# Kernel tuning notes

Hardware: AMD Instinct MI355X
Metric: run time of the kernel (lower is better)

Reference implementation:

```python
import jax, jax.numpy as jnp
import numpy as np

H = 1024   # hidden_dim
I = 256    # input_dim
T = 128    # time_step
NW = 4     # input_num (weeks)
N = 100    # stocks = 5 categories * 20
C, G = 5, 20


def gru(x, Wih, Whh, bih, bhh):
    """Torch-style single-layer GRU. x: (B,T,I) batch_first -> (B,T,H). Gate order r,z,n."""
    gx = jnp.einsum('bti,gi->btg', x, Wih) + bih  # (B,T,3H) input projections precomputed
    h0 = jnp.zeros((x.shape[0], Whh.shape[1]), x.dtype)

    def step(h, g):
        gh = h @ Whh.T + bhh
        xr, xz, xn = jnp.split(g, 3, axis=-1)
        hr, hz, hn = jnp.split(gh, 3, axis=-1)
        r = jax.nn.sigmoid(xr + hr)
        z = jax.nn.sigmoid(xz + hz)
        n = jnp.tanh(xn + r * hn)
        h = (1.0 - z) * n + z * h
        return h, h

    _, ys = jax.lax.scan(step, h0, jnp.swapaxes(gx, 0, 1))
    return jnp.swapaxes(ys, 0, 1)


def att_block(x, W, b):
    """AttentionBlock: x (B,T,D); Linear over time axis, softmax over time, weighted sum."""
    xt = jnp.swapaxes(x, 1, 2)                    # (B,D,T)
    probs = jax.nn.softmax(xt @ W.T + b, axis=-1) # (B,D,T)
    probs = jnp.swapaxes(probs, 1, 2)             # (B,T,D)
    return (probs * x).sum(axis=1)                # (B,D)


def gat(x, edges, W, a_s, a_d, bias):
    """PyG GATConv, heads=1, add_self_loops=True, leaky_relu slope 0.2."""
    n = x.shape[0]
    h = x @ W.T                                   # (n,H)
    loop = jnp.arange(n)
    src = jnp.concatenate([edges[0], loop])
    dst = jnp.concatenate([edges[1], loop])
    e = jax.nn.leaky_relu((h @ a_s)[src] + (h @ a_d)[dst], 0.2)
    m = jax.ops.segment_max(e, dst, num_segments=n)
    ex = jnp.exp(e - m[dst])
    s = jax.ops.segment_sum(ex, dst, num_segments=n)
    alpha = ex / s[dst]
    return jax.ops.segment_sum(alpha[:, None] * h[src], dst, num_segments=n) + bias


def setup_inputs() -> dict:
    key = jax.random.key(0)
    ks = iter(jax.random.split(key, 64))
    p = lambda *s: jax.random.normal(next(ks), s, dtype=jnp.float32) * 0.05
    inp = {}
    for i in range(NW):
        inp[f'w{i}'] = jax.random.normal(next(ks), (N, T, I), dtype=jnp.float32)
    inp['inner_edge'] = jax.random.randint(next(ks), (2, 2000), 0, N, dtype=jnp.int32)
    inp['outer_edge'] = jax.random.randint(next(ks), (2, 25), 0, C, dtype=jnp.int32)
    # per-week sequence encoders (stacked)
    inp['enc_Wih'] = p(NW, 3 * H, I); inp['enc_Whh'] = p(NW, 3 * H, H)
    inp['enc_bih'] = p(NW, 3 * H);    inp['enc_bhh'] = p(NW, 3 * H)
    inp['enc_attW'] = p(NW, T, T);    inp['enc_attb'] = p(NW, T)
    # weekly GRU (not batch_first in torch!)
    inp['wk_Wih'] = p(3 * H, H); inp['wk_Whh'] = p(3 * H, H)
    inp['wk_bih'] = p(3 * H);    inp['wk_bhh'] = p(3 * H)
    inp['wkatt_W'] = p(NW, NW); inp['wkatt_b'] = p(NW)
    inp['pool_W'] = p(G, G);    inp['pool_b'] = p(G)
    inp['ig_W'] = p(H, H); inp['ig_as'] = p(H); inp['ig_ad'] = p(H); inp['ig_b'] = p(H)
    inp['cg_W'] = p(H, H); inp['cg_as'] = p(H); inp['cg_ad'] = p(H); inp['cg_b'] = p(H)
    inp['fus_W'] = p(H, 3 * H); inp['fus_b'] = p(H)
    inp['reg_W'] = p(1, H); inp['reg_b'] = p(1)
    inp['cls_W'] = p(1, H); inp['cls_b'] = p(1)
    return inp


def reference(w0, w1, w2, w3, inner_edge, outer_edge,
              enc_Wih, enc_Whh, enc_bih, enc_bhh, enc_attW, enc_attb,
              wk_Wih, wk_Whh, wk_bih, wk_bhh, wkatt_W, wkatt_b,
              pool_W, pool_b, ig_W, ig_as, ig_ad, ig_b,
              cg_W, cg_as, cg_ad, cg_b, fus_W, fus_b,
              reg_W, reg_b, cls_W, cls_b):
    weeks = [w0, w1, w2, w3]
    embs = []
    for i in range(NW):
        seq = gru(weeks[i], enc_Wih[i], enc_Whh[i], enc_bih[i], enc_bhh[i])  # (N,T,H)
        embs.append(att_block(seq, enc_attW[i], enc_attb[i])[:, None, :])    # (N,1,H)
    we = jnp.concatenate(embs, axis=1)                                       # (N,NW,H)
    # torch nn.GRU default seq-major: scans over dim0 (N stocks), batch=NW
    we = jnp.swapaxes(gru(jnp.swapaxes(we, 0, 1), wk_Wih, wk_Whh, wk_bih, wk_bhh), 0, 1)
    wav = att_block(we, wkatt_W, wkatt_b)                                    # (N,H)
    inner = gat(wav, inner_edge, ig_W, ig_as, ig_ad, ig_b).reshape(C, G, -1)
    wav3 = wav.reshape(C, G, -1)
    cat = att_block(wav3, pool_W, pool_b)                                    # (C,H)
    cat = gat(cat, outer_edge, cg_W, cg_as, cg_ad, cg_b)                     # (C,H)
    cat = jnp.broadcast_to(cat[:, None, :], (C, G, cat.shape[-1]))
    f = jnp.concatenate([wav3, cat, inner], axis=-1)                         # (C,G,3H)
    f = jax.nn.relu(f @ fus_W.T + fus_b)
    reg = (f @ reg_W.T + reg_b).reshape(-1)
    cls = jax.nn.sigmoid(f @ cls_W.T + cls_b).reshape(-1)
    return reg, cls
```

## Files before the change

kernel.cpp:

```cpp
#include <hip/hip_runtime.h>
#include <hip/hip_bf16.h>

#define NW 4
#define NST 100
#define TT 128
#define II 256
#define HH 1024
#define H3 3072

typedef _Float16 h8 __attribute__((ext_vector_type(8)));
typedef float f4 __attribute__((ext_vector_type(4)));

__device__ __forceinline__ float sigf(float x) { return 1.0f / (1.0f + __expf(-x)); }
__device__ __forceinline__ float tanhfast(float x) { return 1.0f - 2.0f / (1.0f + __expf(2.0f * x)); }

__device__ __forceinline__ float4 ld_f4_sc1(const float* p) {
    union { unsigned long long u[2]; float4 v; } r;
    r.u[0] = __hip_atomic_load((unsigned long long*)p, __ATOMIC_RELAXED, __HIP_MEMORY_SCOPE_AGENT);
    r.u[1] = __hip_atomic_load((unsigned long long*)p + 1, __ATOMIC_RELAXED, __HIP_MEMORY_SCOPE_AGENT);
    return r.v;
}
__device__ __forceinline__ float ld_f_sc1(const float* p) {
    return __hip_atomic_load((float*)p, __ATOMIC_RELAXED, __HIP_MEMORY_SCOPE_AGENT);
}

__device__ __forceinline__ void spin_wait(unsigned* f, unsigned t) {
    int guard = 0;
    while (__hip_atomic_load(f, __ATOMIC_RELAXED, __HIP_MEMORY_SCOPE_AGENT) <= t) {
        __builtin_amdgcn_s_sleep(1);
        if (++guard > (1 << 20)) break;
    }
}

__global__ void zero_k(float* a, int n) {
    int i = blockIdx.x * 256 + threadIdx.x;
    if (i < n) a[i] = 0.0f;
}

__global__ void convW_k(const float* __restrict__ Whh, const float* __restrict__ Wih,
                        _Float16* __restrict__ Wc) {
    int col = blockIdx.x * 256 + threadIdx.x;
    int r = blockIdx.y;
    int w = blockIdx.z;
    float v = (col < HH) ? Whh[((size_t)w * H3 + r) * HH + col]
                         : Wih[((size_t)w * H3 + r) * II + (col - HH)];
    Wc[((size_t)w * H3 + r) * 1280 + col] = (_Float16)v;
}

__global__ void convWk_k(const float* __restrict__ src, _Float16* __restrict__ dst) {
    int col = blockIdx.x * 256 + threadIdx.x;
    int r = blockIdx.y;
    dst[(size_t)r * HH + col] = (_Float16)src[(size_t)r * HH + col];
}

__global__ void xcvt_k(const float* __restrict__ x0, const float* __restrict__ x1,
                       const float* __restrict__ x2, const float* __restrict__ x3,
                       _Float16* __restrict__ xT) {
    int idx = blockIdx.x * 256 + threadIdx.x;
    int k8 = idx & 31;
    int m  = (idx >> 5) & 127;
    int t  = (idx >> 12) & 127;
    int w  = idx >> 19;
    const float* xw = (w == 0) ? x0 : (w == 1) ? x1 : (w == 2) ? x2 : x3;
    h8 hv = {};
    if (m < NST) {
        const float* s = xw + ((size_t)m * TT + t) * II + k8 * 8;
        float4 fa = *(const float4*)s;
        float4 fb = *(const float4*)(s + 4);
        hv[0] = (_Float16)fa.x; hv[1] = (_Float16)fa.y;
        hv[2] = (_Float16)fa.z; hv[3] = (_Float16)fa.w;
        hv[4] = (_Float16)fb.x; hv[5] = (_Float16)fb.y;
        hv[6] = (_Float16)fb.z; hv[7] = (_Float16)fb.w;
    }
    *(h8*)&xT[(((size_t)w * TT + t) * 128 + m) * II + k8 * 8] = hv;
}

__global__ void wTcvt_k(const float* __restrict__ attW, float* __restrict__ wT) {
    int tp = threadIdx.x;
    int t  = blockIdx.x;
    int w  = blockIdx.y;
    wT[((size_t)w * TT + t) * TT + tp] = attW[((size_t)w * TT + tp) * TT + t];
}

__global__ void convB_k(const float* __restrict__ bih, const float* __restrict__ bhh,
                        float* __restrict__ bc) {
    int j = blockIdx.x * 256 + threadIdx.x;
    int w = blockIdx.y;
    const float* bi = bih + w * H3;
    const float* bh = bhh + w * H3;
    float* o = bc + w * 4096;
    o[j] = bi[j] + bh[j];
    o[1024 + j] = bi[1024 + j] + bh[1024 + j];
    o[2048 + j] = bi[2048 + j];
    o[3072 + j] = bh[2048 + j];
}

#define ENC_LDS_HALFS (40 * 3 * 16 * 32)
#define ENC_LDS_BYTES (ENC_LDS_HALFS * 2)

__global__ __launch_bounds__(256) void enc_fused_k(
    const _Float16* __restrict__ Wc, const float* __restrict__ bc,
    const _Float16* __restrict__ xT,
    _Float16* __restrict__ hhA, _Float16* __restrict__ hhB,
    _Float16* __restrict__ seq, unsigned* flags)
{
    extern __shared__ _Float16 Bs[];

    int id = blockIdx.x;
    int rr = id & 7, qq = id >> 3;
    int w  = rr >> 1;
    int bx = qq * 2 + (rr & 1);
    int j0 = bx * 16;

    const _Float16* Wcw = Wc + (size_t)w * H3 * 1280;
    const float* bcw = bc + w * 4096;
    _Float16* hA = hhA + (size_t)w * 128 * HH;
    _Float16* hB = hhB + (size_t)w * 128 * HH;
    unsigned* fw = flags + (size_t)w * 64 * 16;
    unsigned* genw = flags + (size_t)(256 + w) * 16;

    int tid = threadIdx.x;
    int lane = tid & 63, wi = tid >> 6, quad = lane >> 4, l15 = lane & 15;

    if (tid < 192) {
        int brow = tid >> 2, bseg = tid & 3;
        int g = brow >> 4, jj = brow & 15;
        const _Float16* bsrc =
            Wcw + (size_t)(g * 1024 + j0 + jj) * 1280 + bseg * 8;
        #pragma unroll 8
        for (int c = 0; c < 40; c++) {
            uint4 v = *(const uint4*)(bsrc + c * 32);
            *(uint4*)&Bs[(((size_t)c * 3 + g) * 16 + jj) * 32 + bseg * 8] = v;
        }
    }
    __syncthreads();

    int j = j0 + l15;
    float br = bcw[j], bz = bcw[1024 + j], bni = bcw[2048 + j], bnh = bcw[3072 + j];
    int r0 = wi * 32 + l15, r1 = wi * 32 + 16 + l15;
    float hreg[2][4] = {};

    h8 xb0[8], xb1[8];
    {
        const _Float16* x0p = xT + ((size_t)w * TT) * 128 * II;
        #pragma unroll
        for (int u = 0; u < 8; u++) {
            xb0[u] = *(const h8*)(x0p + (size_t)r0 * II + quad * 8 + u * 32);
            xb1[u] = *(const h8*)(x0p + (size_t)r1 * II + quad * 8 + u * 32);
        }
    }

    for (int t = 0; t < TT; t++) {
        const _Float16* hin = (t & 1) ? hB : hA;
        _Float16* hout = (t & 1) ? hA : hB;
        const _Float16* pA0h = hin + (size_t)r0 * HH + quad * 8;
        const _Float16* pA1h = hin + (size_t)r1 * HH + quad * 8;

        f4 aR[2] = {}, aZ[2] = {}, aNH[2] = {}, aNX[2] = {};

        h8 rb0[12], rb1[12];
        #pragma unroll
        for (int u = 0; u < 12; u++) {
            rb0[u] = *(const h8*)(pA0h + u * 32);
            rb1[u] = *(const h8*)(pA1h + u * 32);
        }

        #pragma unroll
        for (int c = 0; c < 40; c++) {
            h8 a0, a1;
            if (c < 32) {
                int u = c % 12;
                a0 = rb0[u]; a1 = rb1[u];
                int cn = c + 12;
                if (cn < 32) {
                    rb0[u] = *(const h8*)(pA0h + cn * 32);
                    rb1[u] = *(const h8*)(pA1h + cn * 32);
                }
            } else {
                a0 = xb0[c - 32]; a1 = xb1[c - 32];
            }
            const _Float16* bb = &Bs[(size_t)c * 1536];
            h8 bf0 = *(const h8*)&bb[l15 * 32 + quad * 8];
            h8 bf1 = *(const h8*)&bb[512 + l15 * 32 + quad * 8];
            h8 bf2 = *(const h8*)&bb[1024 + l15 * 32 + quad * 8];
            aR[0] = __builtin_amdgcn_mfma_f32_16x16x32_f16(a0, bf0, aR[0], 0, 0, 0);
            aR[1] = __builtin_amdgcn_mfma_f32_16x16x32_f16(a1, bf0, aR[1], 0, 0, 0);
            aZ[0] = __builtin_amdgcn_mfma_f32_16x16x32_f16(a0, bf1, aZ[0], 0, 0, 0);
            aZ[1] = __builtin_amdgcn_mfma_f32_16x16x32_f16(a1, bf1, aZ[1], 0, 0, 0);
            if (c < 32) {
                aNH[0] = __builtin_amdgcn_mfma_f32_16x16x32_f16(a0, bf2, aNH[0], 0, 0, 0);
                aNH[1] = __builtin_amdgcn_mfma_f32_16x16x32_f16(a1, bf2, aNH[1], 0, 0, 0);
            } else {
                aNX[0] = __builtin_amdgcn_mfma_f32_16x16x32_f16(a0, bf2, aNX[0], 0, 0, 0);
                aNX[1] = __builtin_amdgcn_mfma_f32_16x16x32_f16(a1, bf2, aNX[1], 0, 0, 0);
            }
        }

        unsigned pks[2][4];
        #pragma unroll
        for (int mi = 0; mi < 2; mi++) {
            #pragma unroll
            for (int p = 0; p < 4; p++) {
                int row = wi * 32 + mi * 16 + quad * 4 + p;
                float r = sigf(aR[mi][p] + br);
                float z = sigf(aZ[mi][p] + bz);
                float n = tanhfast(aNX[mi][p] + bni + r * (aNH[mi][p] + bnh));
                float hv = (1.f - z) * n + z * hreg[mi][p];
                hreg[mi][p] = hv;
                unsigned short hb = __builtin_bit_cast(unsigned short, (_Float16)hv);
                unsigned ob = __shfl_xor((unsigned)hb, 1);
                unsigned pk = (unsigned)hb | (ob << 16);
                pks[mi][p] = pk;
                if (!(l15 & 1) && t < TT - 1)
                    __hip_atomic_exchange((unsigned*)&hout[(size_t)row * HH + j], pk,
                                          __ATOMIC_RELAXED, __HIP_MEMORY_SCOPE_AGENT);
            }
        }
        if (t < TT - 1) {
            __syncthreads();
            if (tid == 0)
                __hip_atomic_store(&fw[bx * 16], (unsigned)(t + 1),
                                   __ATOMIC_RELAXED, __HIP_MEMORY_SCOPE_AGENT);
        }
        #pragma unroll
        for (int mi = 0; mi < 2; mi++) {
            #pragma unroll
            for (int p = 0; p < 4; p++) {
                int row = wi * 32 + mi * 16 + quad * 4 + p;
                if (!(l15 & 1) && row < NST)
                    __hip_atomic_store(
                        (unsigned*)&seq[(((size_t)w * NST + row) * TT + t) * HH + j],
                        pks[mi][p], __ATOMIC_RELAXED, __HIP_MEMORY_SCOPE_AGENT);
            }
        }
        if (t < TT - 1) {
            const _Float16* xn = xT + ((size_t)w * TT + t + 1) * 128 * II;
            #pragma unroll
            for (int u = 0; u < 8; u++) {
                xb0[u] = *(const h8*)(xn + (size_t)r0 * II + quad * 8 + u * 32);
                xb1[u] = *(const h8*)(xn + (size_t)r1 * II + quad * 8 + u * 32);
            }
            if (bx == 0) {
                if (tid < 64) spin_wait(&fw[tid * 16], (unsigned)t);
                __syncthreads();
                if (tid == 0)
                    __hip_atomic_store(genw, (unsigned)(t + 1),
                                       __ATOMIC_RELAXED, __HIP_MEMORY_SCOPE_AGENT);
            } else {
                if (tid == 0) spin_wait(genw, (unsigned)t);
                __syncthreads();
            }
            __builtin_amdgcn_fence(__ATOMIC_ACQUIRE, "agent");
        }
    }
}

__global__ __launch_bounds__(256) void att1_k(
    const _Float16* __restrict__ seq, const float* __restrict__ wT,
    const float* __restrict__ attb, float* __restrict__ wex)
{
    int d0 = blockIdx.x * 128;
    int n  = blockIdx.y;
    int w  = blockIdx.z;
    __shared__ _Float16 S[128][128];
    __shared__ float PM[16][136];
    int tid = threadIdx.x;
    const _Float16* sp = seq + ((size_t)(w * NST + n) * TT) * HH + d0;
    for (int q = tid; q < 2048; q += 256) {
        int t = q >> 4, seg = q & 15;
        *(h8*)&S[t][seg * 8] = *(const h8*)(sp + (size_t)t * HH + seg * 8);
    }
    __syncthreads();
    int tx = tid & 15, ty = tid >> 4;
    const float* Wg = wT + (size_t)w * TT * TT;
    float acc[8][8];
    #pragma unroll
    for (int i = 0; i < 8; i++) {
        float b = attb[w * TT + ty * 8 + i];
        for (int j = 0; j < 8; j++) acc[i][j] = b;
    }
    for (int t = 0; t < 128; t++) {
        float wv[8], sv[8];
        float4 wa = *(const float4*)&Wg[(size_t)t * TT + ty * 8];
        float4 wb = *(const float4*)&Wg[(size_t)t * TT + ty * 8 + 4];
        wv[0] = wa.x; wv[1] = wa.y; wv[2] = wa.z; wv[3] = wa.w;
        wv[4] = wb.x; wv[5] = wb.y; wv[6] = wb.z; wv[7] = wb.w;
        h8 s8 = *(const h8*)&S[t][tx * 8];
        #pragma unroll
        for (int j = 0; j < 8; j++) sv[j] = (float)s8[j];
        #pragma unroll
        for (int i = 0; i < 8; i++)
            #pragma unroll
            for (int j = 0; j < 8; j++) acc[i][j] += wv[i] * sv[j];
    }
    float cmax[8], csum[8];
    #pragma unroll
    for (int j = 0; j < 8; j++) {
        float m = acc[0][j];
        for (int i = 1; i < 8; i++) m = fmaxf(m, acc[i][j]);
        PM[ty][tx * 8 + j] = m;
    }
    __syncthreads();
    #pragma unroll
    for (int j = 0; j < 8; j++) {
        float m = -1e30f;
        for (int yy = 0; yy < 16; yy++) m = fmaxf(m, PM[yy][tx * 8 + j]);
        cmax[j] = m;
    }
    __syncthreads();
    #pragma unroll
    for (int j = 0; j < 8; j++) {
        float s = 0.f;
        for (int i = 0; i < 8; i++) { acc[i][j] = expf(acc[i][j] - cmax[j]); s += acc[i][j]; }
        PM[ty][tx * 8 + j] = s;
    }
    __syncthreads();
    #pragma unroll
    for (int j = 0; j < 8; j++) {
        float s = 0.f;
        for (int yy = 0; yy < 16; yy++) s += PM[yy][tx * 8 + j];
        csum[j] = s;
    }
    __syncthreads();
    #pragma unroll
    for (int i = 0; i < 8; i++) {
        h8 s8 = *(const h8*)&S[ty * 8 + i][tx * 8];
        #pragma unroll
        for (int j = 0; j < 8; j++) {
            if (i == 0) PM[ty][tx * 8 + j] = 0.f;
            PM[ty][tx * 8 + j] += acc[i][j] * (float)s8[j];
        }
    }
    __syncthreads();
    if (ty == 0) {
        #pragma unroll
        for (int j = 0; j < 8; j++) {
            float o = 0.f;
            for (int yy = 0; yy < 16; yy++) o += PM[yy][tx * 8 + j];
            wex[((size_t)w * NST + n) * HH + d0 + tx * 8 + j] = o / csum[j];
        }
    }
}

template <int RELU>
__global__ __launch_bounds__(256) void gemm_tn_k(
    const float* __restrict__ A, const float* __restrict__ B,
    const float* __restrict__ bias, float* __restrict__ C, int M, int N, int K)
{
    int n0 = blockIdx.x * 64, m0 = blockIdx.y * 64;
    __shared__ float As[16][64], Bs[16][64];
    int tid = threadIdx.x, tx = tid & 15, ty = tid >> 4;
    float acc[4][4] = {{0.f}};
    for (int k0 = 0; k0 < K; k0 += 16) {
        __syncthreads();
        for (int q = tid; q < 1024; q += 256) {
            int kk = q & 15, r = q >> 4;
            int m = m0 + r, nn = n0 + r;
            As[kk][r] = (m < M) ? A[(size_t)m * K + k0 + kk] : 0.f;
            Bs[kk][r] = (nn < N) ? B[(size_t)nn * K + k0 + kk] : 0.f;
        }
        __syncthreads();
        #pragma unroll
        for (int kk = 0; kk < 16; kk++) {
            float4 av = *(const float4*)&As[kk][ty * 4];
            float4 bv = *(const float4*)&Bs[kk][tx * 4];
            float a[4] = {av.x, av.y, av.z, av.w};
            float b[4] = {bv.x, bv.y, bv.z, bv.w};
            #pragma unroll
            for (int r = 0; r < 4; r++)
                #pragma unroll
                for (int c = 0; c < 4; c++) acc[r][c] += a[r] * b[c];
        }
    }
    #pragma unroll
    for (int r = 0; r < 4; r++) {
        int m = m0 + ty * 4 + r;
        if (m >= M) continue;
        #pragma unroll
        for (int c = 0; c < 4; c++) {
            int nn = n0 + tx * 4 + c;
            if (nn >= N) continue;
            float v = acc[r][c] + (bias ? bias[nn] : 0.f);
            if (RELU) v = fmaxf(v, 0.f);
            C[(size_t)m * N + nn] = v;
        }
    }
}

__global__ __launch_bounds__(256) void wk_fused_k(
    const float* __restrict__ gxw, const _Float16* __restrict__ wkW,
    const float* __restrict__ bhh, float* __restrict__ hA,
    float* __restrict__ hB, float* __restrict__ we2, unsigned* flags)
{
    int tid = threadIdx.x;
    int wi = tid >> 6, lane = tid & 63;
    int j = blockIdx.x * 4 + wi;
    int k0 = lane * 16;
    unsigned* gen = flags + 256 * 16;
    float wf[3][16];
    #pragma unroll
    for (int g = 0; g < 3; g++) {
        h8 wa = *(const h8*)&wkW[(size_t)(g * HH + j) * HH + k0];
        h8 wb = *(const h8*)&wkW[(size_t)(g * HH + j) * HH + k0 + 8];
        #pragma unroll
        for (int i = 0; i < 8; i++) { wf[g][i] = (float)wa[i]; wf[g][8 + i] = (float)wb[i]; }
    }
    float b0 = bhh[j], b1 = bhh[HH + j], b2 = bhh[2 * HH + j];

    for (int t = 0; t < NST; t++) {
        const float* hin = (t & 1) ? hB : hA;
        float* hout = (t & 1) ? hA : hB;
        float acc[4][3] = {};
        #pragma unroll
        for (int b = 0; b < 4; b++) {
            float hv[16];
            #pragma unroll
            for (int s = 0; s < 4; s++) {
                float4 hq = ld_f4_sc1(&hin[b * HH + k0 + s * 4]);
                hv[s * 4] = hq.x; hv[s * 4 + 1] = hq.y;
                hv[s * 4 + 2] = hq.z; hv[s * 4 + 3] = hq.w;
            }
            #pragma unroll
            for (int g = 0; g < 3; g++)
                #pragma unroll
                for (int i = 0; i < 16; i++) acc[b][g] += wf[g][i] * hv[i];
        }
        #pragma unroll
        for (int b = 0; b < 4; b++)
            #pragma unroll
            for (int g = 0; g < 3; g++)
                for (int o = 32; o; o >>= 1) acc[b][g] += __shfl_down(acc[b][g], o);
        if (lane == 0) {
            for (int b = 0; b < 4; b++) {
                const float* gx = gxw + ((size_t)b * NST + t) * H3;
                float hr = acc[b][0] + b0;
                float hz = acc[b][1] + b1;
                float hn = acc[b][2] + b2;
                float r = sigf(gx[j] + hr);
                float z = sigf(gx[HH + j] + hz);
                float n = tanhfast(gx[2 * HH + j] + r * hn);
                float hv = (1.f - z) * n + z * ld_f_sc1(&hin[b * HH + j]);
                __hip_atomic_exchange(&hout[b * HH + j], hv,
                                      __ATOMIC_RELAXED, __HIP_MEMORY_SCOPE_AGENT);
                we2[((size_t)t * 4 + b) * HH + j] = hv;
            }
        }
        if (t < NST - 1) {
            __syncthreads();
            if (tid == 0)
                __hip_atomic_store(&flags[blockIdx.x * 16], (unsigned)(t + 1),
                                   __ATOMIC_RELAXED, __HIP_MEMORY_SCOPE_AGENT);
            if (blockIdx.x == 0) {
                spin_wait(&flags[tid * 16], (unsigned)t);
                __syncthreads();
                if (tid == 0)
                    __hip_atomic_store(gen, (unsigned)(t + 1),
                                       __ATOMIC_RELAXED, __HIP_MEMORY_SCOPE_AGENT);
            } else {
                if (tid == 0) spin_wait(gen, (unsigned)t);
                __syncthreads();
            }
        }
    }
}

__global__ void wkatt_k(const float* __restrict__ we2, const float* __restrict__ W,
                        const float* __restrict__ bv, float* __restrict__ wav)
{
    int n = blockIdx.x;
    for (int d = threadIdx.x; d < HH; d += 256) {
        float v[4], l[4];
        #pragma unroll
        for (int tp = 0; tp < 4; tp++) v[tp] = we2[((size_t)n * 4 + tp) * HH + d];
        float mx = -1e30f;
        #pragma unroll
        for (int tp = 0; tp < 4; tp++) {
            float s = bv[tp];
            for (int t2 = 0; t2 < 4; t2++) s += v[t2] * W[tp * 4 + t2];
            l[tp] = s; mx = fmaxf(mx, s);
        }
        float se = 0.f, o = 0.f;
        #pragma unroll
        for (int tp = 0; tp < 4; tp++) {
            float e = expf(l[tp] - mx);
            se += e; o += e * v[tp];
        }
        wav[(size_t)n * HH + d] = o / se;
    }
}

__global__ void poolatt_k(const float* __restrict__ wav, const float* __restrict__ W,
                          const float* __restrict__ bv, float* __restrict__ cat1)
{
    int c = blockIdx.x;
    for (int d = threadIdx.x; d < HH; d += 256) {
        float v[20], l[20];
        for (int t2 = 0; t2 < 20; t2++) v[t2] = wav[((size_t)c * 20 + t2) * HH + d];
        float mx = -1e30f;
        for (int tp = 0; tp < 20; tp++) {
            float s = bv[tp];
            for (int t2 = 0; t2 < 20; t2++) s += v[t2] * W[tp * 20 + t2];
            l[tp] = s; mx = fmaxf(mx, s);
        }
        float se = 0.f, o = 0.f;
        for (int tp = 0; tp < 20; tp++) {
            float e = expf(l[tp] - mx);
            se += e; o += e * v[tp];
        }
        cat1[(size_t)c * HH + d] = o / se;
    }
}

__global__ void gat_dots_k(const float* __restrict__ h, const float* __restrict__ as_,
                           const float* __restrict__ ad_, float* __restrict__ ss,
                           float* __restrict__ sd)
{
    int i = blockIdx.x, tid = threadIdx.x;
    float s1 = 0.f, s2 = 0.f;
    for (int k = tid; k < HH; k += 256) {
        float v = h[(size_t)i * HH + k];
        s1 += v * as_[k]; s2 += v * ad_[k];
    }
    __shared__ float r1[256], r2[256];
    r1[tid] = s1; r2[tid] = s2; __syncthreads();
    for (int s = 128; s; s >>= 1) {
        if (tid < s) { r1[tid] += r1[tid + s]; r2[tid] += r2[tid + s]; }
        __syncthreads();
    }
    if (tid == 0) { ss[i] = r1[0]; sd[i] = r2[0]; }
}

#define MAXE 256
__global__ __launch_bounds__(256) void gat_agg_k(
    const float* __restrict__ hmat, const int* __restrict__ esrc,
    const int* __restrict__ edst, int nedges, const float* __restrict__ ss,
    const float* __restrict__ sd, const float* __restrict__ bias, float* __restrict__ outp)
{
    int i = blockIdx.x, tid = threadIdx.x;
    __shared__ int cnt;
    __shared__ int msrc[MAXE];
    __shared__ float mw[MAXE];
    __shared__ float inv_s;
    if (tid == 0) {
        cnt = 1; msrc[0] = i;
        float e = ss[i] + sd[i];
        mw[0] = e > 0.f ? e : 0.2f * e;
    }
    __syncthreads();
    for (int e = tid; e < nedges; e += 256) {
        if (edst[e] == i) {
            int p = atomicAdd(&cnt, 1);
            if (p < MAXE) {
                int s = esrc[e];
                msrc[p] = s;
                float v = ss[s] + sd[i];
                mw[p] = v > 0.f ? v : 0.2f * v;
            }
        }
    }
    __syncthreads();
    int m = min(cnt, MAXE);
    if (tid == 0) {
        float mx = -1e30f;
        for (int p = 0; p < m; p++) mx = fmaxf(mx, mw[p]);
        float s = 0.f;
        for (int p = 0; p < m; p++) { float e = expf(mw[p] - mx); mw[p] = e; s += e; }
        inv_s = 1.0f / s;
    }
    __syncthreads();
    for (int d = tid; d < HH; d += 256) {
        float a = 0.f;
        for (int p = 0; p < m; p++) a += mw[p] * hmat[(size_t)msrc[p] * HH + d];
        outp[(size_t)i * HH + d] = a * inv_s + bias[d];
    }
}

__global__ void concat_k(const float* __restrict__ wav, const float* __restrict__ gc,
                         const float* __restrict__ gi, float* __restrict__ cc)
{
    int row = blockIdx.x;
    int c = row / 20;
    for (int k = threadIdx.x; k < H3; k += 256) {
        float v;
        if (k < HH) v = wav[(size_t)row * HH + k];
        else if (k < 2 * HH) v = gc[(size_t)c * HH + (k - HH)];
        else v = gi[(size_t)row * HH + (k - 2 * HH)];
        cc[(size_t)row * H3 + k] = v;
    }
}

__global__ void heads_k(const float* __restrict__ f, const float* __restrict__ regW,
                        const float* __restrict__ regb, const float* __restrict__ clsW,
                        const float* __restrict__ clsb, float* __restrict__ outp)
{
    int i = blockIdx.x, tid = threadIdx.x;
    float s1 = 0.f, s2 = 0.f;
    for (int k = tid; k < HH; k += 256) {
        float v = f[(size_t)i * HH + k];
        s1 += v * regW[k]; s2 += v * clsW[k];
    }
    __shared__ float r1[256], r2[256];
    r1[tid] = s1; r2[tid] = s2; __syncthreads();
    for (int s = 128; s; s >>= 1) {
        if (tid < s) { r1[tid] += r1[tid + s]; r2[tid] += r2[tid + s]; }
        __syncthreads();
    }
    if (tid == 0) {
        outp[i] = r1[0] + regb[0];
        outp[100 + i] = sigf(r2[0] + clsb[0]);
    }
}

extern "C" void kernel_launch(void* const* d_in, const int* in_sizes, int n_in,
                              void* d_out, int out_size, void* d_ws, size_t ws_size,
                              hipStream_t stream)
{
    (void)in_sizes; (void)n_in; (void)out_size; (void)ws_size;
    const float* x0 = (const float*)d_in[0];
    const float* x1 = (const float*)d_in[1];
    const float* x2 = (const float*)d_in[2];
    const float* x3 = (const float*)d_in[3];
    const int*   ie = (const int*)d_in[4];
    const int*   oe = (const int*)d_in[5];
    const float* enc_Wih = (const float*)d_in[6];
    const float* enc_Whh = (const float*)d_in[7];
    const float* enc_bih = (const float*)d_in[8];
    const float* enc_bhh = (const float*)d_in[9];
    const float* enc_attW = (const float*)d_in[10];
    const float* enc_attb = (const float*)d_in[11];
    const float* wk_Wih = (const float*)d_in[12];
    const float* wk_Whh = (const float*)d_in[13];
    const float* wk_bih = (const float*)d_in[14];
    const float* wk_bhh = (const float*)d_in[15];
    const float* wkatt_W = (const float*)d_in[16];
    const float* wkatt_b = (const float*)d_in[17];
    const float* pool_W = (const float*)d_in[18];
    const float* pool_b = (const float*)d_in[19];
    const float* ig_W = (const float*)d_in[20];
    const float* ig_as = (const float*)d_in[21];
    const float* ig_ad = (const float*)d_in[22];
    const float* ig_b = (const float*)d_in[23];
    const float* cg_W = (const float*)d_in[24];
    const float* cg_as = (const float*)d_in[25];
    const float* cg_ad = (const float*)d_in[26];
    const float* cg_b = (const float*)d_in[27];
    const float* fus_W = (const float*)d_in[28];
    const float* fus_b = (const float*)d_in[29];
    const float* reg_W = (const float*)d_in[30];
    const float* reg_b = (const float*)d_in[31];
    const float* cls_W = (const float*)d_in[32];
    const float* cls_b = (const float*)d_in[33];
    float* outp = (float*)d_out;

    char* p = (char*)d_ws;
    auto alloc = [&](size_t bytes) { char* r = p; p += (bytes + 255) & ~(size_t)255; return (void*)r; };
    unsigned* flags = (unsigned*)alloc(1024 * 16 * 4);
    _Float16* Wcat = (_Float16*)alloc((size_t)NW * H3 * 1280 * 2);
    float* bc = (float*)alloc((size_t)NW * 4 * HH * 4);
    _Float16* wkW = (_Float16*)alloc((size_t)H3 * HH * 2);
    _Float16* xT = (_Float16*)alloc((size_t)NW * TT * 128 * II * 2);
    float* wT = (float*)alloc((size_t)NW * TT * TT * 4);
    _Float16* hhA = (_Float16*)alloc((size_t)NW * 128 * HH * 2);
    _Float16* hhB = (_Float16*)alloc((size_t)NW * 128 * HH * 2);
    _Float16* seq = (_Float16*)alloc((size_t)NW * NST * TT * HH * 2);
    float* wex = (float*)alloc((size_t)NW * NST * HH * 4);
    float* gxw = (float*)alloc((size_t)NW * NST * H3 * 4);
    float* hwA = (float*)alloc(4 * HH * 4);
    float* hwB = (float*)alloc(4 * HH * 4);
    float* we2 = (float*)alloc((size_t)NST * 4 * HH * 4);
    float* wav = (float*)alloc((size_t)NST * HH * 4);
    float* hi  = (float*)alloc((size_t)NST * HH * 4);
    float* si_s = (float*)alloc(128 * 4);
    float* si_d = (float*)alloc(128 * 4);
    float* gi  = (float*)alloc((size_t)NST * HH * 4);
    float* cat1 = (float*)alloc(5 * HH * 4);
    float* hc  = (float*)alloc(5 * HH * 4);
    float* sc_s = (float*)alloc(64 * 4);
    float* sc_d = (float*)alloc(64 * 4);
    float* gc  = (float*)alloc(5 * HH * 4);
    float* cc  = (float*)alloc((size_t)NST * H3 * 4);
    float* fbuf = (float*)alloc((size_t)NST * HH * 4);

    static bool attr_done = false;
    if (!attr_done) {
        hipFuncSetAttribute((const void*)enc_fused_k,
                            hipFuncAttributeMaxDynamicSharedMemorySize, ENC_LDS_BYTES);
        attr_done = true;
    }

    zero_k<<<64, 256, 0, stream>>>((float*)flags, 1024 * 16);
    convW_k<<<dim3(5, H3, NW), 256, 0, stream>>>(enc_Whh, enc_Wih, Wcat);
    convB_k<<<dim3(4, NW), 256, 0, stream>>>(enc_bih, enc_bhh, bc);
    convWk_k<<<dim3(4, H3), 256, 0, stream>>>(wk_Whh, wkW);
    xcvt_k<<<8192, 256, 0, stream>>>(x0, x1, x2, x3, xT);
    wTcvt_k<<<dim3(TT, NW), 128, 0, stream>>>(enc_attW, wT);
    zero_k<<<(NW * 128 * HH / 2 + 255) / 256, 256, 0, stream>>>((float*)hhA, NW * 128 * HH / 2);
    zero_k<<<(4 * HH + 255) / 256, 256, 0, stream>>>(hwA, 4 * HH);

    enc_fused_k<<<256, 256, ENC_LDS_BYTES, stream>>>(
        Wcat, bc, xT, hhA, hhB, seq, flags);

    att1_k<<<dim3(8, NST, NW), 256, 0, stream>>>(seq, wT, enc_attb, wex);

    gemm_tn_k<0><<<dim3(48, 7), 256, 0, stream>>>(wex, wk_Wih, wk_bih, gxw, 400, H3, HH);

    wk_fused_k<<<256, 256, 0, stream>>>(gxw, wkW, wk_bhh, hwA, hwB, we2, flags + 512 * 16);

    wkatt_k<<<NST, 256, 0, stream>>>(we2, wkatt_W, wkatt_b, wav);

    gemm_tn_k<0><<<dim3(16, 2), 256, 0, stream>>>(wav, ig_W, nullptr, hi, NST, HH, HH);
    gat_dots_k<<<NST, 256, 0, stream>>>(hi, ig_as, ig_ad, si_s, si_d);
    gat_agg_k<<<NST, 256, 0, stream>>>(hi, ie, ie + 2000, 2000, si_s, si_d, ig_b, gi);

    poolatt_k<<<5, 256, 0, stream>>>(wav, pool_W, pool_b, cat1);
    gemm_tn_k<0><<<dim3(16, 1), 256, 0, stream>>>(cat1, cg_W, nullptr, hc, 5, HH, HH);
    gat_dots_k<<<5, 256, 0, stream>>>(hc, cg_as, cg_ad, sc_s, sc_d);
    gat_agg_k<<<5, 256, 0, stream>>>(hc, oe, oe + 25, 25, sc_s, sc_d, cg_b, gc);

    concat_k<<<NST, 256, 0, stream>>>(wav, gc, gi, cc);
    gemm_tn_k<1><<<dim3(16, 2), 256, 0, stream>>>(cc, fus_W, fus_b, fbuf, NST, HH, H3);
    heads_k<<<NST, 256, 0, stream>>>(fbuf, reg_W, reg_b, cls_W, cls_b, outp);
}
```

Baseline: 4.599 ms.

## Use MFMA in time-attention kernel, reorder encoder K loop, prefetch week-GRU operands

The time-axis attention kernel now converts the attention weights to fp16 in LDS and computes the logits with 16x16x32 MFMA. The softmax and weighted sum use lane shuffles instead of LDS reductions, and the separate weight-transpose kernel is removed. The encoder GRU step processes the input-projection K chunks first, so those MFMAs can run before the recurrent hidden-state loads arrive. The week GRU loads its hidden state and gate inputs before the dot-product loop rather than after the reduction. Together these target the scalar FP32 attention cost and latency on the serial recurrent path, at the cost of fp16 precision in the attention weights.

```diff
diff --git a/kernel.cpp b/kernel.cpp
--- a/kernel.cpp
+++ b/kernel.cpp
@@ -75,13 +75,6 @@
     *(h8*)&xT[(((size_t)w * TT + t) * 128 + m) * II + k8 * 8] = hv;
 }
 
-__global__ void wTcvt_k(const float* __restrict__ attW, float* __restrict__ wT) {
-    int tp = threadIdx.x;
-    int t  = blockIdx.x;
-    int w  = blockIdx.y;
-    wT[((size_t)w * TT + t) * TT + tp] = attW[((size_t)w * TT + tp) * TT + t];
-}
-
 __global__ void convB_k(const float* __restrict__ bih, const float* __restrict__ bhh,
                         float* __restrict__ bc) {
     int j = blockIdx.x * 256 + threadIdx.x;
@@ -166,9 +159,12 @@
         }
 
         #pragma unroll
-        for (int c = 0; c < 40; c++) {
+        for (int cc = 0; cc < 40; cc++) {
+            int c = (cc < 8) ? (32 + cc) : (cc - 8);
             h8 a0, a1;
-            if (c < 32) {
+            if (c >= 32) {
+                a0 = xb0[c - 32]; a1 = xb1[c - 32];
+            } else {
                 int u = c % 12;
                 a0 = rb0[u]; a1 = rb1[u];
                 int cn = c + 12;
@@ -176,8 +172,6 @@
                     rb0[u] = *(const h8*)(pA0h + cn * 32);
                     rb1[u] = *(const h8*)(pA1h + cn * 32);
                 }
-            } else {
-                a0 = xb0[c - 32]; a1 = xb1[c - 32];
             }
             const _Float16* bb = &Bs[(size_t)c * 1536];
             h8 bf0 = *(const h8*)&bb[l15 * 32 + quad * 8];
@@ -256,88 +250,96 @@
 }
 
 __global__ __launch_bounds__(256) void att1_k(
-    const _Float16* __restrict__ seq, const float* __restrict__ wT,
+    const _Float16* __restrict__ seq, const float* __restrict__ attW,
     const float* __restrict__ attb, float* __restrict__ wex)
 {
     int d0 = blockIdx.x * 128;
     int n  = blockIdx.y;
     int w  = blockIdx.z;
     __shared__ _Float16 S[128][128];
-    __shared__ float PM[16][136];
+    __shared__ _Float16 Wh[128][128];
     int tid = threadIdx.x;
     const _Float16* sp = seq + ((size_t)(w * NST + n) * TT) * HH + d0;
     for (int q = tid; q < 2048; q += 256) {
         int t = q >> 4, seg = q & 15;
         *(h8*)&S[t][seg * 8] = *(const h8*)(sp + (size_t)t * HH + seg * 8);
     }
+    const float* Wsrc = attW + (size_t)w * TT * TT;
+    for (int q = tid; q < 2048; q += 256) {
+        int tp = q >> 4, seg = q & 15;
+        const float* s = Wsrc + (size_t)tp * TT + seg * 8;
+        float4 fa = *(const float4*)s;
+        float4 fb = *(const float4*)(s + 4);
+        h8 hv;
+        hv[0] = (_Float16)fa.x; hv[1] = (_Float16)fa.y;
+        hv[2] = (_Float16)fa.z; hv[3] = (_Float16)fa.w;
+        hv[4] = (_Float16)fb.x; hv[5] = (_Float16)fb.y;
+        hv[6] = (_Float16)fb.z; hv[7] = (_Float16)fb.w;
+        *(h8*)&Wh[tp][seg * 8] = hv;
+    }
     __syncthreads();
-    int tx = tid & 15, ty = tid >> 4;
-    const float* Wg = wT + (size_t)w * TT * TT;
-    float acc[8][8];
+
+    int lane = tid & 63, wi = tid >> 6, quad = lane >> 4, l15 = lane & 15;
+
+    h8 af[2][4];
     #pragma unroll
-    for (int i = 0; i < 8; i++) {
-        float b = attb[w * TT + ty * 8 + i];
-        for (int j = 0; j < 8; j++) acc[i][j] = b;
-    }
-    for (int t = 0; t < 128; t++) {
-        float wv[8], sv[8];
-        float4 wa = *(const float4*)&Wg[(size_t)t * TT + ty * 8];
-        float4 wb = *(const float4*)&Wg[(size_t)t * TT + ty * 8 + 4];
-        wv[0] = wa.x; wv[1] = wa.y; wv[2] = wa.z; wv[3] = wa.w;
-        wv[4] = wb.x; wv[5] = wb.y; wv[6] = wb.z; wv[7] = wb.w;
-        h8 s8 = *(const h8*)&S[t][tx * 8];
-        #pragma unroll
-        for (int j = 0; j < 8; j++) sv[j] = (float)s8[j];
-        #pragma unroll
-        for (int i = 0; i < 8; i++)
-            #pragma unroll
-            for (int j = 0; j < 8; j++) acc[i][j] += wv[i] * sv[j];
-    }
-    float cmax[8], csum[8];
+    for (int mi = 0; mi < 2; mi++) {
+        int dl = wi * 32 + mi * 16 + l15;
+        #pragma unroll
+        for (int kc = 0; kc < 4; kc++) {
+            h8 v;
+            #pragma unroll
+            for (int i = 0; i < 8; i++)
+                v[i] = S[kc * 32 + quad * 8 + i][dl];
+            af[mi][kc] = v;
+        }
+    }
+    f4 zero4 = {0.f, 0.f, 0.f, 0.f};
+    f4 acc[2][8];
     #pragma unroll
-    for (int j = 0; j < 8; j++) {
-        float m = acc[0][j];
-        for (int i = 1; i < 8; i++) m = fmaxf(m, acc[i][j]);
-        PM[ty][tx * 8 + j] = m;
-    }
-    __syncthreads();
+    for (int mi = 0; mi < 2; mi++)
+        #pragma unroll
+        for (int ni = 0; ni < 8; ni++) acc[mi][ni] = zero4;
     #pragma unroll
-    for (int j = 0; j < 8; j++) {
-        float m = -1e30f;
-        for (int yy = 0; yy < 16; yy++) m = fmaxf(m, PM[yy][tx * 8 + j]);
-        cmax[j] = m;
-    }
-    __syncthreads();
+    for (int ni = 0; ni < 8; ni++) {
+        #pragma unroll
+        for (int kc = 0; kc < 4; kc++) {
+            h8 bf = *(const h8*)&Wh[ni * 16 + l15][kc * 32 + quad * 8];
+            acc[0][ni] = __builtin_amdgcn_mfma_f32_16x16x32_f16(af[0][kc], bf, acc[0][ni], 0, 0, 0);
+            acc[1][ni] = __builtin_amdgcn_mfma_f32_16x16x32_f16(af[1][kc], bf, acc[1][ni], 0, 0, 0);
+        }
+    }
+    float bias_[8];
     #pragma unroll
-    for (int j = 0; j < 8; j++) {
-        float s = 0.f;
-        for (int i = 0; i < 8; i++) { acc[i][j] = expf(acc[i][j] - cmax[j]); s += acc[i][j]; }
-        PM[ty][tx * 8 + j] = s;
-    }
-    __syncthreads();
+    for (int ni = 0; ni < 8; ni++) bias_[ni] = attb[w * TT + ni * 16 + l15];
+
     #pragma unroll
-    for (int j = 0; j < 8; j++) {
-        float s = 0.f;
-        for (int yy = 0; yy < 16; yy++) s += PM[yy][tx * 8 + j];
-        csum[j] = s;
-    }
-    __syncthreads();
-    #pragma unroll
-    for (int i = 0; i < 8; i++) {
-        h8 s8 = *(const h8*)&S[ty * 8 + i][tx * 8];
-        #pragma unroll
-        for (int j = 0; j < 8; j++) {
-            if (i == 0) PM[ty][tx * 8 + j] = 0.f;
-            PM[ty][tx * 8 + j] += acc[i][j] * (float)s8[j];
-        }
-    }
-    __syncthreads();
-    if (ty == 0) {
-        #pragma unroll
-        for (int j = 0; j < 8; j++) {
-            float o = 0.f;
-            for (int yy = 0; yy < 16; yy++) o += PM[yy][tx * 8 + j];
-            wex[((size_t)w * NST + n) * HH + d0 + tx * 8 + j] = o / csum[j];
+    for (int mi = 0; mi < 2; mi++) {
+        #pragma unroll
+        for (int p = 0; p < 4; p++) {
+            float vle[8];
+            float mx = -1e30f;
+            #pragma unroll
+            for (int ni = 0; ni < 8; ni++) {
+                vle[ni] = acc[mi][ni][p] + bias_[ni];
+                mx = fmaxf(mx, vle[ni]);
+            }
+            #pragma unroll
+            for (int o = 8; o; o >>= 1) mx = fmaxf(mx, __shfl_xor(mx, o, 16));
+            float sm = 0.f;
+            #pragma unroll
+            for (int ni = 0; ni < 8; ni++) { vle[ni] = __expf(vle[ni] - mx); sm += vle[ni]; }
+            #pragma unroll
+            for (int o = 8; o; o >>= 1) sm += __shfl_xor(sm, o, 16);
+            int dl = wi * 32 + mi * 16 + quad * 4 + p;
+            float ps = 0.f;
+            #pragma unroll
+            for (int ni = 0; ni < 8; ni++)
+                ps += vle[ni] * (float)S[ni * 16 + l15][dl];
+            #pragma unroll
+            for (int o = 8; o; o >>= 1) ps += __shfl_xor(ps, o, 16);
+            if (l15 == 0)
+                wex[((size_t)w * NST + n) * HH + d0 + dl] = ps / sm;
         }
     }
 }
@@ -410,6 +412,13 @@
     for (int t = 0; t < NST; t++) {
         const float* hin = (t & 1) ? hB : hA;
         float* hout = (t & 1) ? hA : hB;
+        float hj[4], gxv[4][3];
+        #pragma unroll
+        for (int b = 0; b < 4; b++) {
+            hj[b] = ld_f_sc1(&hin[b * HH + j]);
+            const float* gx = gxw + ((size_t)b * NST + t) * H3;
+            gxv[b][0] = gx[j]; gxv[b][1] = gx[HH + j]; gxv[b][2] = gx[2 * HH + j];
+        }
         float acc[4][3] = {};
         #pragma unroll
         for (int b = 0; b < 4; b++) {
@@ -432,14 +441,13 @@
                 for (int o = 32; o; o >>= 1) acc[b][g] += __shfl_down(acc[b][g], o);
         if (lane == 0) {
             for (int b = 0; b < 4; b++) {
-                const float* gx = gxw + ((size_t)b * NST + t) * H3;
                 float hr = acc[b][0] + b0;
                 float hz = acc[b][1] + b1;
                 float hn = acc[b][2] + b2;
-                float r = sigf(gx[j] + hr);
-                float z = sigf(gx[HH + j] + hz);
-                float n = tanhfast(gx[2 * HH + j] + r * hn);
-                float hv = (1.f - z) * n + z * ld_f_sc1(&hin[b * HH + j]);
+                float r = sigf(gxv[b][0] + hr);
+                float z = sigf(gxv[b][1] + hz);
+                float n = tanhfast(gxv[b][2] + r * hn);
+                float hv = (1.f - z) * n + z * hj[b];
                 __hip_atomic_exchange(&hout[b * HH + j], hv,
                                       __ATOMIC_RELAXED, __HIP_MEMORY_SCOPE_AGENT);
                 we2[((size_t)t * 4 + b) * HH + j] = hv;
@@ -659,7 +667,6 @@
     float* bc = (float*)alloc((size_t)NW * 4 * HH * 4);
     _Float16* wkW = (_Float16*)alloc((size_t)H3 * HH * 2);
     _Float16* xT = (_Float16*)alloc((size_t)NW * TT * 128 * II * 2);
-    float* wT = (float*)alloc((size_t)NW * TT * TT * 4);
     _Float16* hhA = (_Float16*)alloc((size_t)NW * 128 * HH * 2);
     _Float16* hhB = (_Float16*)alloc((size_t)NW * 128 * HH * 2);
     _Float16* seq = (_Float16*)alloc((size_t)NW * NST * TT * HH * 2);
@@ -693,14 +700,13 @@
     convB_k<<<dim3(4, NW), 256, 0, stream>>>(enc_bih, enc_bhh, bc);
     convWk_k<<<dim3(4, H3), 256, 0, stream>>>(wk_Whh, wkW);
     xcvt_k<<<8192, 256, 0, stream>>>(x0, x1, x2, x3, xT);
-    wTcvt_k<<<dim3(TT, NW), 128, 0, stream>>>(enc_attW, wT);
     zero_k<<<(NW * 128 * HH / 2 + 255) / 256, 256, 0, stream>>>((float*)hhA, NW * 128 * HH / 2);
     zero_k<<<(4 * HH + 255) / 256, 256, 0, stream>>>(hwA, 4 * HH);
 
     enc_fused_k<<<256, 256, ENC_LDS_BYTES, stream>>>(
         Wcat, bc, xT, hhA, hhB, seq, flags);
 
-    att1_k<<<dim3(8, NST, NW), 256, 0, stream>>>(seq, wT, enc_attb, wex);
+    att1_k<<<dim3(8, NST, NW), 256, 0, stream>>>(seq, enc_attW, enc_attb, wex);
 
     gemm_tn_k<0><<<dim3(48, 7), 256, 0, stream>>>(wex, wk_Wih, wk_bih, gxw, 400, H3, HH);
 
```

After: 4.385 ms. 4.6% less time.
